# Kernel optimization log

Hardware: AMD Instinct MI355X
Metric: run time of the kernel (lower is better)

The kernel has to match this reference:

```python
import jax, jax.numpy as jnp
import numpy as np

B, T, J, V, D, H = 32, 400, 30, 50000, 150, 150
L = 2  # answer_token_len (boundary model: start, end)


def _gru_step(h, x, Wih, Whh, bih, bhh):
    # torch GRUCell semantics
    gi = x @ Wih.T + bih
    gh = h @ Whh.T + bhh
    ir, iz, inn = jnp.split(gi, 3, axis=-1)
    hr, hz, hn = jnp.split(gh, 3, axis=-1)
    r = jax.nn.sigmoid(ir + hr)
    z = jax.nn.sigmoid(iz + hz)
    n = jnp.tanh(inn + r * hn)
    return (1.0 - z) * n + z * h


def _gru_seq(x, Wih, Whh, bih, bhh):
    # x: [B, S, din] -> hidden sequence [B, S, h]
    h0 = jnp.zeros((x.shape[0], Whh.shape[1]), x.dtype)
    def step(h, xt):
        h = _gru_step(h, xt, Wih, Whh, bih, bhh)
        return h, h
    _, hs = jax.lax.scan(step, h0, jnp.swapaxes(x, 0, 1))
    return jnp.swapaxes(hs, 0, 1)


def _forward(context, query,
             E,
             ctx_Wih, ctx_Whh, ctx_bih, ctx_bhh,
             q_Wih, q_Whh, q_bih, q_bhh,
             Wq, Wp, Wr, w, gate_bias, attn_bias,
             m_Wih, m_Whh, m_bih, m_bhh,
             mr_Wih, mr_Whh, mr_bih, mr_bhh,
             ptr_W1, ptr_W2, ptr_v,
             d_Wih, d_Whh, d_bih, d_bhh):
    # encode context and query with GRUs
    Hp = _gru_seq(E[context], ctx_Wih, ctx_Whh, ctx_bih, ctx_bhh)  # [B,T,H]
    Hq = _gru_seq(E[query], q_Wih, q_Whh, q_bih, q_bhh)            # [B,J,H]

    whq = jnp.einsum('bjh,hk->bjk', Hq, Wq)  # precomputed query projection [B,J,H]

    def match_scan(xs, cWih, cWhh, cbih, cbhh):
        # xs: [B,T,H] context encodings (possibly time-reversed)
        def step(h, xt):
            # G_i = tanh(Wq Hq + (Wp p_i + Wr h_{i-1}) + bias)  -> [B,J,H]
            g = jnp.tanh(whq + (xt @ Wp + h @ Wr + gate_bias)[:, None, :])
            a = jax.nn.softmax(g @ w + attn_bias, axis=-1)       # [B,J]
            q = jnp.einsum('bj,bjh->bh', a, Hq)                  # attended query
            z = jnp.concatenate([xt, q], axis=-1)                # [B,2H]
            h = _gru_step(h, z, cWih, cWhh, cbih, cbhh)
            return h, h
        h0 = jnp.zeros((xs.shape[0], xs.shape[2]), xs.dtype)
        _, hs = jax.lax.scan(step, h0, jnp.swapaxes(xs, 0, 1))
        return jnp.swapaxes(hs, 0, 1)  # [B,T,H]

    Hf = match_scan(Hp, m_Wih, m_Whh, m_bih, m_bhh)              # forward direction
    Hb = match_scan(Hp[:, ::-1], mr_Wih, mr_Whh, mr_bih, mr_bhh) # reverse direction (scan order, as original)
    Hr = jnp.concatenate([Hf, Hb], axis=-1)                      # [B,T,2H]
    zero0 = jnp.zeros((Hr.shape[0], 1, Hr.shape[2]), Hr.dtype)   # initial zero state prepended
    Hr = jnp.concatenate([zero0, Hr], axis=1)                    # [B,T+1,2H]

    # boundary pointer network: L attention steps over H_r
    enc = Hr @ ptr_W1
    def ptr_step(h, _):
        s = jnp.tanh(enc + (h @ ptr_W2)[:, None, :]) @ ptr_v     # [B,T+1]
        a = jax.nn.softmax(s, axis=-1)
        c = jnp.einsum('bt,bth->bh', a, Hr)
        h = _gru_step(h, c, d_Wih, d_Whh, d_bih, d_bhh)
        return h, a
    h0 = jnp.zeros((Hr.shape[0], Hr.shape[2]), Hr.dtype)
    _, probs = jax.lax.scan(ptr_step, h0, None, length=L)
    return jnp.swapaxes(probs, 0, 1)  # [B, L, T+1]


def setup_inputs() -> dict:
    key = jax.random.key(0)
    keys = iter(jax.random.split(key, 40))
    p = lambda *s: jax.random.normal(next(keys), s, jnp.float32) * 0.05
    inp = {
        'context': jax.random.randint(next(keys), (B, T), 0, V, dtype=jnp.int32),
        'query': jax.random.randint(next(keys), (B, J), 0, V, dtype=jnp.int32),
        'E': p(V, D),
        'ctx_Wih': p(3 * H, D), 'ctx_Whh': p(3 * H, H), 'ctx_bih': p(3 * H), 'ctx_bhh': p(3 * H),
        'q_Wih': p(3 * H, D), 'q_Whh': p(3 * H, H), 'q_bih': p(3 * H), 'q_bhh': p(3 * H),
        'Wq': p(H, H), 'Wp': p(H, H), 'Wr': p(H, H), 'w': p(H),
        'gate_bias': p(H), 'attn_bias': p(),
        'm_Wih': p(3 * H, 2 * H), 'm_Whh': p(3 * H, H), 'm_bih': p(3 * H), 'm_bhh': p(3 * H),
        'mr_Wih': p(3 * H, 2 * H), 'mr_Whh': p(3 * H, H), 'mr_bih': p(3 * H), 'mr_bhh': p(3 * H),
        'ptr_W1': p(2 * H, 2 * H), 'ptr_W2': p(2 * H, 2 * H), 'ptr_v': p(2 * H),
        'd_Wih': p(6 * H, 2 * H), 'd_Whh': p(6 * H, 2 * H), 'd_bih': p(6 * H), 'd_bhh': p(6 * H),
    }
    return inp


def reference(context, query, E,
              ctx_Wih, ctx_Whh, ctx_bih, ctx_bhh,
              q_Wih, q_Whh, q_bih, q_bhh,
              Wq, Wp, Wr, w, gate_bias, attn_bias,
              m_Wih, m_Whh, m_bih, m_bhh,
              mr_Wih, mr_Whh, mr_bih, mr_bhh,
              ptr_W1, ptr_W2, ptr_v,
              d_Wih, d_Whh, d_bih, d_bhh):
    return _forward(context, query, E,
                    ctx_Wih, ctx_Whh, ctx_bih, ctx_bhh,
                    q_Wih, q_Whh, q_bih, q_bhh,
                    Wq, Wp, Wr, w, gate_bias, attn_bias,
                    m_Wih, m_Whh, m_bih, m_bhh,
                    mr_Wih, mr_Whh, mr_bih, mr_bhh,
                    ptr_W1, ptr_W2, ptr_v,
                    d_Wih, d_Whh, d_bih, d_bhh)
```

## Files before the change

### kernel.cpp

```cpp
#include <hip/hip_runtime.h>
#include <hip/hip_bf16.h>


namespace {

constexpr int NBATCH = 32;
constexpr int TLEN   = 400;
constexpr int JQ     = 30;
constexpr int T1     = 401;

__device__ __forceinline__ float sigm(float x){ return 1.f/(1.f+__expf(-x)); }
__device__ __forceinline__ float tanh_f(float x){
  float e = __expf(-2.f*fabsf(x));
  float t = (1.f-e)/(1.f+e);
  return x < 0.f ? -t : t;
}
__device__ __forceinline__ float bf2f(unsigned short u){
  union { unsigned int i; float f; } c; c.i = ((unsigned int)u)<<16; return c.f;
}

#define NW 29
struct WDesc { const void* src[NW]; int off[NW+1]; };

__global__ void sniff_kernel(const unsigned int* __restrict__ bits, int* __restrict__ flag){
  __shared__ int cnt;
  if (threadIdx.x==0) cnt = 0;
  __syncthreads();
  int hit = 0;
  #pragma unroll
  for (int i=0;i<4;i++){
    unsigned int w = bits[threadIdx.x*4+i];
    unsigned int b = (w>>8)&0x7Fu;
    if (b==0u || (b>=0x38u && b<=0x3Fu)) hit++;
  }
  atomicAdd(&cnt, hit);
  __syncthreads();
  if (threadIdx.x==0) *flag = (cnt > 768) ? 1 : 0;
}

__global__ void convert_weights_kernel(WDesc d, float* __restrict__ out, const int* __restrict__ flag){
  const int isbf = *flag;
  const int total = d.off[NW];
  for (int e = blockIdx.x*blockDim.x+threadIdx.x; e < total; e += gridDim.x*blockDim.x){
    int j = 0;
    while (e >= d.off[j+1]) j++;
    int i = e - d.off[j];
    out[e] = isbf ? bf2f(((const unsigned short*)d.src[j])[i])
                  : ((const float*)d.src[j])[i];
  }
}

__global__ void padrows_kernel(const float* __restrict__ src, float* __restrict__ dst,
                               int rows, int cols, int ldd){
  int i = blockIdx.x*blockDim.x+threadIdx.x;
  if (i >= rows*ldd) return;
  int r = i/ldd, c = i-r*ldd;
  dst[i] = (c<cols) ? src[(size_t)r*cols+c] : 0.f;
}

__global__ void build_wcat_kernel(const float* __restrict__ Whh, const float* __restrict__ Wr,
                                  float* __restrict__ Wcat){
  int i = blockIdx.x*blockDim.x+threadIdx.x;
  if (i >= 600*152) return;
  int r = i/152, c = i-r*152;
  float v = 0.f;
  if (c < 150){
    if (r < 450) v = Whh[(size_t)r*150+c];
    else         v = Wr[(size_t)c*150 + (r-450)];
  }
  Wcat[i] = v;
}

__global__ void build_msplit_kernel(const float* __restrict__ Wcat,
                                    float* __restrict__ s2q, float* __restrict__ ext){
  int i = blockIdx.x*blockDim.x+threadIdx.x;
  if (i < 24576){
    int q = i/2048, rem = i-q*2048, r = rem/4, p = rem-r*4;
    s2q[i] = Wcat[(size_t)r*152 + 104 + 4*q + p];
  } else if (i < 24576+13376){
    int k = i-24576;
    int q = k/352, rem = k-q*352, ii = rem/4, p = rem-ii*4;
    ext[k] = Wcat[(size_t)(512+ii)*152 + 4*q + p];
  }
}

__global__ void build_gsplit_kernel(const float* __restrict__ Wpad, float* __restrict__ s2q){
  int i = blockIdx.x*blockDim.x+threadIdx.x;
  if (i >= 12*452*4) return;
  int q = i/1808, rem = i-q*1808, r = rem/4, p = rem-r*4;
  s2q[i] = (r<450) ? Wpad[(size_t)r*152 + 104 + 4*q + p] : 0.f;
}

__global__ __launch_bounds__(512) void rowproj_kernel(
    const float* __restrict__ Xrows,
    const int* __restrict__ gather, const void* __restrict__ Etab, const int* __restrict__ bfflag,
    const float* __restrict__ W, const float* __restrict__ bias,
    float* __restrict__ out, int rows, int K, int inner, int mode, int ldw, int offw, int ldo)
{
  __shared__ float xs[8][304];
  const int r0 = blockIdx.x*8;
  int nr = rows - r0; if (nr > 8) nr = 8;
  if (nr <= 0) return;
  const int isbf = gather ? *bfflag : 0;
  for (int e = threadIdx.x; e < nr*inner; e += blockDim.x){
    int r = e/inner, i = e - r*inner;
    float v;
    if (gather){
      size_t base = (size_t)gather[r0+r]*inner + i;
      v = isbf ? bf2f(((const unsigned short*)Etab)[base]) : ((const float*)Etab)[base];
    } else {
      v = Xrows[(size_t)(r0+r)*inner + i];
    }
    xs[r][i] = v;
  }
  __syncthreads();
  for (int k = threadIdx.x; k < ldo; k += blockDim.x){
    if (k < K){
      float b0 = bias ? bias[k] : 0.f;
      float acc[8];
      #pragma unroll
      for (int r=0;r<8;r++) acc[r] = b0;
      if (mode==0){
        for (int i=0;i<inner;i++){
          float wv = W[(size_t)i*ldw + k];
          #pragma unroll
          for (int r=0;r<8;r++) acc[r] += xs[r][i]*wv;
        }
      } else {
        const float* wr = W + (size_t)k*ldw + offw;
        for (int i=0;i<inner;i++){
          float wv = wr[i];
          #pragma unroll
          for (int r=0;r<8;r++) acc[r] += xs[r][i]*wv;
        }
      }
      for (int r=0;r<nr;r++) out[(size_t)(r0+r)*ldo + k] = acc[r];
    } else {
      for (int r=0;r<nr;r++) out[(size_t)(r0+r)*ldo + k] = 0.f;
    }
  }
}

#define R26(M) M(0) M(1) M(2) M(3) M(4) M(5) M(6) M(7) M(8) M(9) M(10) M(11) \
               M(12) M(13) M(14) M(15) M(16) M(17) M(18) M(19) M(20) M(21) \
               M(22) M(23) M(24) M(25)
#define DECW(i) float4 w##i;
#define LDW(i)  w##i = wrow4[i];
#define FMAW(i) { float4 hq = h4[i]; \
  acc0 = fmaf(hq.x, w##i.x, acc0); acc1 = fmaf(hq.y, w##i.y, acc1); \
  acc0 = fmaf(hq.z, w##i.z, acc0); acc1 = fmaf(hq.w, w##i.w, acc1); }

__global__ __launch_bounds__(512) void gru_scan_kernel(
    const float* __restrict__ gi0, const float* __restrict__ Wp0,
    const float* __restrict__ s2q0, const float* __restrict__ bh0,
    float* __restrict__ H0, int S0,
    const float* __restrict__ gi1, const float* __restrict__ Wp1,
    const float* __restrict__ s2q1, const float* __restrict__ bh1,
    float* __restrict__ H1, int S1)
{
  const int blk = blockIdx.x;
  const float* gi; const float* Wpad; const float* s2qG; const float* bh; float* Hs; int S;
  if (blk < 32){ gi = gi0 + (size_t)blk*S0*450;  Wpad = Wp0; s2qG = s2q0; bh = bh0;
                 Hs = H0 + (size_t)blk*S0*150;   S = S0; }
  else         { int bb = blk-32;
                 gi = gi1 + (size_t)bb*S1*450;   Wpad = Wp1; s2qG = s2q1; bh = bh1;
                 Hs = H1 + (size_t)bb*S1*150;    S = S1; }
  __shared__ float4 s2W[12*452];
  __shared__ __align__(16) float h[152];
  __shared__ float gh[452];
  const int tid = threadIdx.x;

  R26(DECW)
  float br = 0.f;
  {
    const float4* wrow4 = (const float4*)(Wpad + (size_t)((tid<450)?tid:0)*152);
    R26(LDW)
    if (tid<450) br = bh[tid];
  }
  for (int e=tid; e<12*452; e+=512) s2W[e] = ((const float4*)s2qG)[e];
  if (tid < 152) h[tid] = 0.f;
  __syncthreads();
  const float4* h4 = (const float4*)h;

  for (int t=0;t<S;t++){
    float g0=0.f,g1=0.f,g2=0.f;
    if (tid < 150){
      const float* gg = gi + (size_t)t*450;
      g0 = gg[tid]; g1 = gg[150+tid]; g2 = gg[300+tid];
    }
    if (tid < 450){
      float acc0=br, acc1=0.f;
      R26(FMAW)
      #pragma unroll
      for (int q=0;q<12;q++){
        float4 wq = s2W[q*452+tid]; float4 hq = h4[26+q];
        acc0 = fmaf(hq.x, wq.x, acc0); acc1 = fmaf(hq.y, wq.y, acc1);
        acc0 = fmaf(hq.z, wq.z, acc0); acc1 = fmaf(hq.w, wq.w, acc1);
      }
      gh[tid] = acc0+acc1;
    }
    __syncthreads();
    if (tid < 150){
      float r = sigm(g0 + gh[tid]);
      float z = sigm(g1 + gh[150+tid]);
      float n = tanh_f(g2 + r*gh[300+tid]);
      float hn = (1.f-z)*n + z*h[tid];
      h[tid] = hn;
      Hs[(size_t)t*150 + tid] = hn;
    }
    __syncthreads();
  }
}

__global__ void zero_hr0_kernel(float* __restrict__ Hr){
  int idx = blockIdx.x*blockDim.x + threadIdx.x;
  if (idx < NBATCH*300){
    int b = idx/300, k = idx - 300*b;
    Hr[(size_t)b*T1*300 + k] = 0.f;
  }
}

__global__ __launch_bounds__(512) void match_scan_kernel(
    const float* __restrict__ pWp,
    const float* __restrict__ whq,
    const float* __restrict__ giXf,
    const float* __restrict__ giXr,
    const float* __restrict__ Pf,
    const float* __restrict__ Pr,
    const float* __restrict__ WcatF, const float* __restrict__ WcatR,
    const float* __restrict__ s2qF,  const float* __restrict__ s2qR,
    const float* __restrict__ extF,  const float* __restrict__ extR,
    const float* __restrict__ m_bhh, const float* __restrict__ mr_bhh,
    const float* __restrict__ wvec,
    float* __restrict__ Hr)
{
  const int b   = blockIdx.x;
  const int dir = blockIdx.y;
  const float* giX  = dir ? giXr : giXf;
  const float* P    = dir ? Pr   : Pf;
  const float* Wcat = dir ? WcatR : WcatF;
  const float* s2qG = dir ? s2qR  : s2qF;
  const float* extG = dir ? extR  : extF;
  const float* bhh  = dir ? mr_bhh : m_bhh;

  __shared__ float4 s2W[12*512];
  __shared__ float4 extW[38*88];
  __shared__ float4 uS[339];
  __shared__ __align__(16) float h[152];
  __shared__ float ghsRaw[512];
  __shared__ __align__(16) float base[152];
  __shared__ __align__(16) float gis[452];
  __shared__ __align__(16) float pwS[152];
  __shared__ __align__(16) float wlS[152];
  __shared__ float sc[32], attw[32];

  const int tid  = threadIdx.x;
  const int lane = tid & 63;
  const int wv   = tid >> 6;
  const int er   = (tid < 440) ? (tid % 88) : 0;
  const int kg   = (tid < 440) ? (tid / 88) : 0;
  const int dq   = (tid < 339) ? (tid % 113) : 0;
  const int djg  = (tid < 339) ? (tid / 113) : 0;

  R26(DECW)
  float br;
  {
    const float4* wrow4 = (const float4*)(Wcat + (size_t)tid*152);
    R26(LDW)
    br = (tid < 450) ? bhh[tid] : 0.f;
  }
  for (int e=tid; e<12*512; e+=512) s2W[e]  = ((const float4*)s2qG)[e];
  for (int e=tid; e<38*88;  e+=512) extW[e] = ((const float4*)extG)[e];
  if (tid < 152){
    h[tid] = 0.f;
    base[tid] = 0.f;
    wlS[tid] = (tid<150) ? wvec[tid] : 0.f;
  }
  __syncthreads();
  const float4* h4 = (const float4*)h;

  for (int t=0;t<TLEN;t++){
    const int tt = dir ? (TLEN-1-t) : t;

    {
      float acc0=br, acc1=0.f;
      R26(FMAW)
      #pragma unroll
      for (int q=0;q<12;q++){
        float4 wq = s2W[q*512+tid]; float4 hq = h4[26+q];
        acc0 = fmaf(hq.x, wq.x, acc0); acc1 = fmaf(hq.y, wq.y, acc1);
        acc0 = fmaf(hq.z, wq.z, acc0); acc1 = fmaf(hq.w, wq.w, acc1);
      }
      ghsRaw[tid] = acc0+acc1;
    }
    if (tid < 440){
      float e0=0.f, e1=0.f;
      #pragma unroll
      for (int j=0;j<8;j++){
        int q = kg*8+j;
        if (q < 38){
          float4 wq = extW[q*88+er]; float4 hq = h4[q];
          e0 = fmaf(hq.x, wq.x, e0); e1 = fmaf(hq.y, wq.y, e1);
          e0 = fmaf(hq.z, wq.z, e0); e1 = fmaf(hq.w, wq.w, e1);
        }
      }
      ((float*)uS)[kg*96+er] = e0+e1;
    } else if (tid < 478){
      int u = tid-440;
      ((float4*)pwS)[u] = ((const float4*)(pWp + ((size_t)b*TLEN + tt)*152))[u];
    }
    __syncthreads();

    if (tid < 150){
      float v = pwS[tid];
      if (tid < 62) v += ghsRaw[450+tid];
      else {
        int k = tid-62;
        const float* pS = (const float*)uS;
        v += pS[k] + pS[96+k] + pS[192+k] + pS[288+k] + pS[384+k];
      }
      base[tid] = v;
    }
    __syncthreads();

    #pragma unroll
    for (int jj=0;jj<4;jj++){
      int j = wv + 8*jj;
      float a = 0.f;
      if (j < JQ && lane < 38){
        float4 q4 = ((const float4*)(whq + ((size_t)b*JQ + j)*152))[lane];
        float4 b4 = ((const float4*)base)[lane];
        float4 w4 = ((const float4*)wlS)[lane];
        a = w4.x*tanh_f(q4.x+b4.x);
        a = fmaf(w4.y, tanh_f(q4.y+b4.y), a);
        a = fmaf(w4.z, tanh_f(q4.z+b4.z), a);
        a = fmaf(w4.w, tanh_f(q4.w+b4.w), a);
      }
      #pragma unroll
      for (int off=32; off; off>>=1) a += __shfl_down(a, off);
      if (j < JQ && lane==0) sc[j] = a;
    }
    __syncthreads();

    if (tid < 64){
      float v = (tid < JQ) ? sc[tid] : -1e30f;
      float m = v;
      #pragma unroll
      for (int off=32; off; off>>=1) m = fmaxf(m, __shfl_down(m, off));
      m = __shfl(m, 0);
      float e = (tid < JQ) ? __expf(v-m) : 0.f;
      float su = e;
      #pragma unroll
      for (int off=32; off; off>>=1) su += __shfl_down(su, off);
      su = __shfl(su, 0);
      if (tid < JQ) attw[tid] = e/su;
    }
    __syncthreads();

    if (tid < 339){
      const float4* P4 = (const float4*)(P + ((size_t)b*JQ + djg*10)*452) + dq;
      float4 a; a.x=0.f; a.y=0.f; a.z=0.f; a.w=0.f;
      #pragma unroll 2
      for (int j=0;j<10;j++){
        float aw = attw[djg*10+j];
        float4 p = P4[(size_t)j*113];
        a.x = fmaf(aw, p.x, a.x); a.y = fmaf(aw, p.y, a.y);
        a.z = fmaf(aw, p.z, a.z); a.w = fmaf(aw, p.w, a.w);
      }
      uS[djg*113+dq] = a;
    }
    __syncthreads();

    if (tid < 113){
      float4 gq = ((const float4*)(giX + ((size_t)b*TLEN + tt)*452))[tid];
      float4 d0 = uS[tid], d1 = uS[113+tid], d2 = uS[226+tid];
      gq.x += d0.x+d1.x+d2.x; gq.y += d0.y+d1.y+d2.y;
      gq.z += d0.z+d1.z+d2.z; gq.w += d0.w+d1.w+d2.w;
      ((float4*)gis)[tid] = gq;
    }
    __syncthreads();

    if (tid < 150){
      float r = sigm(gis[tid] + ghsRaw[tid]);
      float z = sigm(gis[150+tid] + ghsRaw[150+tid]);
      float n = tanh_f(gis[300+tid] + r*ghsRaw[300+tid]);
      float hn = (1.f-z)*n + z*h[tid];
      h[tid] = hn;
      Hr[((size_t)b*T1 + (t+1))*300 + dir*150 + tid] = hn;
    }
    __syncthreads();
  }
}

__global__ __launch_bounds__(512,2) void ptr_scan_kernel(
    const float* __restrict__ enc, const float* __restrict__ Hr,
    const float* __restrict__ W2, const float* __restrict__ pv,
    const float* __restrict__ dWih, const float* __restrict__ dWhh,
    const float* __restrict__ dbih, const float* __restrict__ dbhh,
    void* __restrict__ outv, const int* __restrict__ flag)
{
  const int b = blockIdx.x;
  const int tid = threadIdx.x;
  const int isbf = *flag;
  __shared__ float h[300], hW2[300], sl[T1], al[T1], c[300];
  __shared__ float gis[900], ghs[900];
  __shared__ float vl[300];
  __shared__ float red[8];
  if (tid < 300){ h[tid] = 0.f; vl[tid] = pv[tid]; }
  __syncthreads();
  for (int l=0;l<2;l++){
    if (tid < 300){
      float a0=0.f,a1=0.f;
      for (int i=0;i<300;i+=2){
        a0 += h[i]  *W2[(size_t)i*300+tid];
        a1 += h[i+1]*W2[(size_t)(i+1)*300+tid];
      }
      hW2[tid] = a0+a1;
    }
    __syncthreads();
    {
      const int wv = tid>>6, lane = tid&63;
      for (int t=wv; t<T1; t+=8){
        const float* er = enc + ((size_t)b*T1 + t)*300;
        float acc = 0.f;
        for (int k=lane; k<300; k+=64) acc += vl[k]*tanh_f(er[k] + hW2[k]);
        #pragma unroll
        for (int off=32; off; off>>=1) acc += __shfl_down(acc, off);
        if (lane==0) sl[t] = acc;
      }
    }
    __syncthreads();
    {
      float v = (tid < T1) ? sl[tid] : -1e30f;
      float m = v;
      #pragma unroll
      for (int off=32; off; off>>=1) m = fmaxf(m, __shfl_down(m, off));
      if ((tid&63)==0) red[tid>>6] = m;
      __syncthreads();
      float bm = fmaxf(fmaxf(fmaxf(red[0],red[1]),fmaxf(red[2],red[3])),
                       fmaxf(fmaxf(red[4],red[5]),fmaxf(red[6],red[7])));
      float e = (tid < T1) ? __expf(v-bm) : 0.f;
      float su = e;
      #pragma unroll
      for (int off=32; off; off>>=1) su += __shfl_down(su, off);
      __syncthreads();
      if ((tid&63)==0) red[tid>>6] = su;
      __syncthreads();
      float bs = red[0]+red[1]+red[2]+red[3]+red[4]+red[5]+red[6]+red[7];
      if (tid < T1){
        float a = e/bs;
        al[tid] = a;
        size_t oi = ((size_t)b*2 + l)*T1 + tid;
        if (isbf) ((__hip_bfloat16*)outv)[oi] = __float2bfloat16(a);
        else      ((float*)outv)[oi] = a;
      }
    }
    __syncthreads();
    if (tid < 300){
      float acc = 0.f;
      for (int t=0;t<T1;t++) acc += al[t]*Hr[((size_t)b*T1 + t)*300 + tid];
      c[tid] = acc;
    }
    __syncthreads();
    for (int k=tid; k<900; k+=blockDim.x){
      const float* wi = dWih + (size_t)k*300;
      const float* wh = dWhh + (size_t)k*300;
      float a0 = dbih[k], a1 = dbhh[k];
      for (int i=0;i<300;i++){ a0 += c[i]*wi[i]; a1 += h[i]*wh[i]; }
      gis[k] = a0; ghs[k] = a1;
    }
    __syncthreads();
    if (tid < 300){
      float r = sigm(gis[tid] + ghs[tid]);
      float z = sigm(gis[300+tid] + ghs[300+tid]);
      float n = tanh_f(gis[600+tid] + r*ghs[600+tid]);
      h[tid] = (1.f-z)*n + z*h[tid];
    }
    __syncthreads();
  }
}

}

extern "C" void kernel_launch(void* const* d_in, const int* in_sizes, int n_in,
                              void* d_out, int out_size, void* d_ws, size_t ws_size,
                              hipStream_t stream)
{
  (void)in_sizes; (void)n_in; (void)out_size; (void)ws_size;
  float* ws = (float*)d_ws;
  int* flag = (int*)d_ws;

  static const int wsz[NW] = {
    67500,67500,450,450,
    67500,67500,450,450,
    22500,22500,22500,150,150,1,
    135000,67500,450,450,
    135000,67500,450,450,
    90000,90000,300,
    270000,270000,900,900
  };
  WDesc desc;
  int cum = 0;
  for (int j=0;j<NW;j++){ desc.src[j] = d_in[3+j]; desc.off[j] = cum; cum += wsz[j]; }
  desc.off[NW] = cum;

  float* WB = ws + 16;
  const float* P_ctx_Wih = WB + desc.off[0];
  const float* P_ctx_Whh = WB + desc.off[1];
  const float* P_ctx_bih = WB + desc.off[2];
  const float* P_ctx_bhh = WB + desc.off[3];
  const float* P_q_Wih   = WB + desc.off[4];
  const float* P_q_Whh   = WB + desc.off[5];
  const float* P_q_bih   = WB + desc.off[6];
  const float* P_q_bhh   = WB + desc.off[7];
  const float* P_Wq      = WB + desc.off[8];
  const float* P_Wp      = WB + desc.off[9];
  const float* P_Wr      = WB + desc.off[10];
  const float* P_w       = WB + desc.off[11];
  const float* P_gb      = WB + desc.off[12];
  const float* P_m_Wih   = WB + desc.off[14];
  const float* P_m_Whh   = WB + desc.off[15];
  const float* P_m_bih   = WB + desc.off[16];
  const float* P_m_bhh   = WB + desc.off[17];
  const float* P_mr_Wih  = WB + desc.off[18];
  const float* P_mr_Whh  = WB + desc.off[19];
  const float* P_mr_bih  = WB + desc.off[20];
  const float* P_mr_bhh  = WB + desc.off[21];
  const float* P_W1      = WB + desc.off[22];
  const float* P_W2      = WB + desc.off[23];
  const float* P_pv      = WB + desc.off[24];
  const float* P_dWih    = WB + desc.off[25];
  const float* P_dWhh    = WB + desc.off[26];
  const float* P_dbih    = WB + desc.off[27];
  const float* P_dbhh    = WB + desc.off[28];

  size_t p = 16 + 1468512;
  float* ctxWhhP = ws + p; p += 68400;
  float* qWhhP   = ws + p; p += 68400;
  float* s2qCtx  = ws + p; p += 21696;
  float* s2qQ    = ws + p; p += 21696;
  float* WcatF   = ws + p; p += 91200;
  float* WcatR   = ws + p; p += 91200;
  float* s2qF    = ws + p; p += 24576;
  float* s2qR    = ws + p; p += 24576;
  float* extFg   = ws + p; p += 13376;
  float* extRg   = ws + p; p += 13376;

  float* ctx_gi = ws + p; p += 5760000;
  float* q_gi   = ws + p; p += 432000;
  float* HpB    = ws + p; p += 1920000;
  float* HqB    = ws + p; p += 144000;
  float* whqB   = ws + p; p += 145920;
  float* PfB    = ws + p; p += 433920;
  float* PrB    = ws + p; p += 433920;
  float* pWpB   = ws + p; p += 1945600;
  float* giXfB  = ws + p; p += 5785600;
  float* giXrB  = ws + p; p += 5785600;
  float* HrB    = ws + p; p += 3849600;
  float* encB   = ctx_gi;

  sniff_kernel<<<1,256,0,stream>>>((const unsigned int*)d_in[2], flag);
  convert_weights_kernel<<<512,256,0,stream>>>(desc, WB, flag);
  padrows_kernel<<<(450*152+255)/256,256,0,stream>>>(P_ctx_Whh, ctxWhhP, 450,150,152);
  padrows_kernel<<<(450*152+255)/256,256,0,stream>>>(P_q_Whh,   qWhhP,   450,150,152);
  build_gsplit_kernel<<<(12*452*4+255)/256,256,0,stream>>>(ctxWhhP, s2qCtx);
  build_gsplit_kernel<<<(12*452*4+255)/256,256,0,stream>>>(qWhhP,   s2qQ);
  build_wcat_kernel<<<(600*152+255)/256,256,0,stream>>>(P_m_Whh,  P_Wr, WcatF);
  build_wcat_kernel<<<(600*152+255)/256,256,0,stream>>>(P_mr_Whh, P_Wr, WcatR);
  build_msplit_kernel<<<(24576+13376+255)/256,256,0,stream>>>(WcatF, s2qF, extFg);
  build_msplit_kernel<<<(24576+13376+255)/256,256,0,stream>>>(WcatR, s2qR, extRg);

  rowproj_kernel<<<1600,512,0,stream>>>(nullptr,(const int*)d_in[0], d_in[2], flag,
                                        P_ctx_Wih, P_ctx_bih, ctx_gi, 12800,450,150,1,150,0,450);
  rowproj_kernel<<<120,512,0,stream>>>(nullptr,(const int*)d_in[1], d_in[2], flag,
                                       P_q_Wih, P_q_bih, q_gi, 960,450,150,1,150,0,450);

  gru_scan_kernel<<<64,512,0,stream>>>(ctx_gi, ctxWhhP, s2qCtx, P_ctx_bhh, HpB, 400,
                                       q_gi,   qWhhP,   s2qQ,   P_q_bhh,   HqB, 30);

  rowproj_kernel<<<120,192,0,stream>>>(HqB,nullptr,nullptr,nullptr, P_Wq, nullptr,
                                       whqB, 960,150,150,0,150,0,152);
  rowproj_kernel<<<120,512,0,stream>>>(HqB,nullptr,nullptr,nullptr, P_m_Wih, nullptr,
                                       PfB, 960,450,150,1,300,150,452);
  rowproj_kernel<<<120,512,0,stream>>>(HqB,nullptr,nullptr,nullptr, P_mr_Wih, nullptr,
                                       PrB, 960,450,150,1,300,150,452);
  rowproj_kernel<<<1600,192,0,stream>>>(HpB,nullptr,nullptr,nullptr, P_Wp, P_gb,
                                        pWpB, 12800,150,150,0,150,0,152);
  rowproj_kernel<<<1600,512,0,stream>>>(HpB,nullptr,nullptr,nullptr, P_m_Wih, P_m_bih,
                                        giXfB, 12800,450,150,1,300,0,452);
  rowproj_kernel<<<1600,512,0,stream>>>(HpB,nullptr,nullptr,nullptr, P_mr_Wih, P_mr_bih,
                                        giXrB, 12800,450,150,1,300,0,452);

  zero_hr0_kernel<<<(NBATCH*300+511)/512,512,0,stream>>>(HrB);
  match_scan_kernel<<<dim3(NBATCH,2),512,0,stream>>>(pWpB, whqB, giXfB, giXrB,
                                                     PfB, PrB, WcatF, WcatR,
                                                     s2qF, s2qR, extFg, extRg,
                                                     P_m_bhh, P_mr_bhh, P_w, HrB);

  rowproj_kernel<<<1604,320,0,stream>>>(HrB,nullptr,nullptr,nullptr, P_W1, nullptr,
                                        encB, 12832,300,300,0,300,0,300);
  ptr_scan_kernel<<<32,512,0,stream>>>(encB, HrB, P_W2, P_pv,
                                       P_dWih, P_dWhh, P_dbih, P_dbhh, d_out, flag);
}
```

Measured before the change: 3.643 ms.

## Batch multiple sequences per block in GRU and match scans to reuse weights

The GRU encoder scan now handles four batch rows per block (16 blocks instead of 64), and the match scan handles two batch rows per block (32 blocks instead of 64). Register- and LDS-resident recurrent weights are reused across the rows, so each weight load feeds several FMAs. The match scan's phases are restructured: the full attention-weighted sum over j is done in one pass, and several syncs and partial-sum buffers are removed. In exchange, far fewer blocks run on a large GPU and the serial per-step latency grows, which is a risk in these latency-bound recurrent loops.

Result: slower. 8.469 ms (+132.5%).

```diff
diff --git a/kernel.cpp b/kernel.cpp
--- a/kernel.cpp
+++ b/kernel.cpp
@@ -146,9 +146,16 @@
                M(22) M(23) M(24) M(25)
 #define DECW(i) float4 w##i;
 #define LDW(i)  w##i = wrow4[i];
-#define FMAW(i) { float4 hq = h4[i]; \
-  acc0 = fmaf(hq.x, w##i.x, acc0); acc1 = fmaf(hq.y, w##i.y, acc1); \
-  acc0 = fmaf(hq.z, w##i.z, acc0); acc1 = fmaf(hq.w, w##i.w, acc1); }
+#define FMAW2(i) { float4 p = h04[i]; float4 r2 = h14[i]; \
+  a0 = fmaf(p.x,  w##i.x, a0); a1 = fmaf(p.y,  w##i.y, a1); \
+  a0 = fmaf(p.z,  w##i.z, a0); a1 = fmaf(p.w,  w##i.w, a1); \
+  c0 = fmaf(r2.x, w##i.x, c0); c1 = fmaf(r2.y, w##i.y, c1); \
+  c0 = fmaf(r2.z, w##i.z, c0); c1 = fmaf(r2.w, w##i.w, c1); }
+#define FMAW4(i) { float4 p0=hA4[i], p1=hB4[i], p2=hC4[i], p3=hD4[i]; \
+  a0=fmaf(p0.x,w##i.x,a0); a0=fmaf(p0.y,w##i.y,a0); a0=fmaf(p0.z,w##i.z,a0); a0=fmaf(p0.w,w##i.w,a0); \
+  a1=fmaf(p1.x,w##i.x,a1); a1=fmaf(p1.y,w##i.y,a1); a1=fmaf(p1.z,w##i.z,a1); a1=fmaf(p1.w,w##i.w,a1); \
+  a2=fmaf(p2.x,w##i.x,a2); a2=fmaf(p2.y,w##i.y,a2); a2=fmaf(p2.z,w##i.z,a2); a2=fmaf(p2.w,w##i.w,a2); \
+  a3=fmaf(p3.x,w##i.x,a3); a3=fmaf(p3.y,w##i.y,a3); a3=fmaf(p3.z,w##i.z,a3); a3=fmaf(p3.w,w##i.w,a3); }
 
 __global__ __launch_bounds__(512) void gru_scan_kernel(
     const float* __restrict__ gi0, const float* __restrict__ Wp0,
@@ -160,53 +167,73 @@
 {
   const int blk = blockIdx.x;
   const float* gi; const float* Wpad; const float* s2qG; const float* bh; float* Hs; int S;
-  if (blk < 32){ gi = gi0 + (size_t)blk*S0*450;  Wpad = Wp0; s2qG = s2q0; bh = bh0;
-                 Hs = H0 + (size_t)blk*S0*150;   S = S0; }
-  else         { int bb = blk-32;
-                 gi = gi1 + (size_t)bb*S1*450;   Wpad = Wp1; s2qG = s2q1; bh = bh1;
-                 Hs = H1 + (size_t)bb*S1*150;    S = S1; }
-  __shared__ float4 s2W[12*452];
-  __shared__ __align__(16) float h[152];
-  __shared__ float gh[452];
+  if (blk < 8){ int b0 = 4*blk;
+    gi = gi0 + (size_t)b0*S0*450;  Wpad = Wp0; s2qG = s2q0; bh = bh0;
+    Hs = H0 + (size_t)b0*S0*150;   S = S0;
+  } else { int b0 = 4*(blk-8);
+    gi = gi1 + (size_t)b0*S1*450;  Wpad = Wp1; s2qG = s2q1; bh = bh1;
+    Hs = H1 + (size_t)b0*S1*150;   S = S1;
+  }
+  __shared__ float4 s2W[5424];
+  __shared__ __align__(16) float hg[4][152];
+  __shared__ float ghB[4][452];
   const int tid = threadIdx.x;
 
   R26(DECW)
-  float br = 0.f;
+  float br;
   {
     const float4* wrow4 = (const float4*)(Wpad + (size_t)((tid<450)?tid:0)*152);
     R26(LDW)
-    if (tid<450) br = bh[tid];
-  }
-  for (int e=tid; e<12*452; e+=512) s2W[e] = ((const float4*)s2qG)[e];
-  if (tid < 152) h[tid] = 0.f;
+    br = (tid<450) ? bh[tid] : 0.f;
+  }
+  for (int e=tid; e<5424; e+=512) s2W[e] = ((const float4*)s2qG)[e];
+  if (tid < 152){ hg[0][tid]=0.f; hg[1][tid]=0.f; hg[2][tid]=0.f; hg[3][tid]=0.f; }
   __syncthreads();
-  const float4* h4 = (const float4*)h;
+  const float4* hA4 = (const float4*)hg[0];
+  const float4* hB4 = (const float4*)hg[1];
+  const float4* hC4 = (const float4*)hg[2];
+  const float4* hD4 = (const float4*)hg[3];
+
+  const int bb1 = tid/150;
+  const int k1  = tid - 150*bb1;
 
   for (int t=0;t<S;t++){
-    float g0=0.f,g1=0.f,g2=0.f;
-    if (tid < 150){
-      const float* gg = gi + (size_t)t*450;
-      g0 = gg[tid]; g1 = gg[150+tid]; g2 = gg[300+tid];
-    }
+    const float* gg = gi + ((size_t)(bb1*S) + t)*450 + k1;
+    float g0 = gg[0], g1 = gg[150], g2 = gg[300];
+
     if (tid < 450){
-      float acc0=br, acc1=0.f;
-      R26(FMAW)
+      float a0=br, a1=br, a2=br, a3=br;
+      R26(FMAW4)
       #pragma unroll
       for (int q=0;q<12;q++){
-        float4 wq = s2W[q*452+tid]; float4 hq = h4[26+q];
-        acc0 = fmaf(hq.x, wq.x, acc0); acc1 = fmaf(hq.y, wq.y, acc1);
-        acc0 = fmaf(hq.z, wq.z, acc0); acc1 = fmaf(hq.w, wq.w, acc1);
-      }
-      gh[tid] = acc0+acc1;
-    }
-    __syncthreads();
-    if (tid < 150){
-      float r = sigm(g0 + gh[tid]);
-      float z = sigm(g1 + gh[150+tid]);
-      float n = tanh_f(g2 + r*gh[300+tid]);
-      float hn = (1.f-z)*n + z*h[tid];
-      h[tid] = hn;
-      Hs[(size_t)t*150 + tid] = hn;
+        float4 wq = s2W[q*452+tid];
+        float4 p0=hA4[26+q], p1=hB4[26+q], p2=hC4[26+q], p3=hD4[26+q];
+        a0=fmaf(p0.x,wq.x,a0); a0=fmaf(p0.y,wq.y,a0); a0=fmaf(p0.z,wq.z,a0); a0=fmaf(p0.w,wq.w,a0);
+        a1=fmaf(p1.x,wq.x,a1); a1=fmaf(p1.y,wq.y,a1); a1=fmaf(p1.z,wq.z,a1); a1=fmaf(p1.w,wq.w,a1);
+        a2=fmaf(p2.x,wq.x,a2); a2=fmaf(p2.y,wq.y,a2); a2=fmaf(p2.z,wq.z,a2); a2=fmaf(p2.w,wq.w,a2);
+        a3=fmaf(p3.x,wq.x,a3); a3=fmaf(p3.y,wq.y,a3); a3=fmaf(p3.z,wq.z,a3); a3=fmaf(p3.w,wq.w,a3);
+      }
+      ghB[0][tid]=a0; ghB[1][tid]=a1; ghB[2][tid]=a2; ghB[3][tid]=a3;
+    }
+    __syncthreads();
+
+    {
+      float r = sigm(g0 + ghB[bb1][k1]);
+      float z = sigm(g1 + ghB[bb1][150+k1]);
+      float n = tanh_f(g2 + r*ghB[bb1][300+k1]);
+      float hn = (1.f-z)*n + z*hg[bb1][k1];
+      hg[bb1][k1] = hn;
+      Hs[((size_t)(bb1*S) + t)*150 + k1] = hn;
+    }
+    if (tid < 88){
+      int k2 = 62 + tid;
+      const float* g2p = gi + ((size_t)(3*S) + t)*450 + k2;
+      float r = sigm(g2p[0]   + ghB[3][k2]);
+      float z = sigm(g2p[150] + ghB[3][150+k2]);
+      float n = tanh_f(g2p[300] + r*ghB[3][300+k2]);
+      float hn = (1.f-z)*n + z*hg[3][k2];
+      hg[3][k2] = hn;
+      Hs[((size_t)(3*S) + t)*150 + k2] = hn;
     }
     __syncthreads();
   }
@@ -234,7 +261,7 @@
     const float* __restrict__ wvec,
     float* __restrict__ Hr)
 {
-  const int b   = blockIdx.x;
+  const int b0  = blockIdx.x*2;
   const int dir = blockIdx.y;
   const float* giX  = dir ? giXr : giXf;
   const float* P    = dir ? Pr   : Pf;
@@ -243,24 +270,19 @@
   const float* extG = dir ? extR  : extF;
   const float* bhh  = dir ? mr_bhh : m_bhh;
 
-  __shared__ float4 s2W[12*512];
-  __shared__ float4 extW[38*88];
-  __shared__ float4 uS[339];
-  __shared__ __align__(16) float h[152];
-  __shared__ float ghsRaw[512];
-  __shared__ __align__(16) float base[152];
-  __shared__ __align__(16) float gis[452];
-  __shared__ __align__(16) float pwS[152];
+  __shared__ float4 s2W[6144];
+  __shared__ float4 extW[3344];
+  __shared__ __align__(16) float h[2][152];
+  __shared__ float ghsB[2][512];
+  __shared__ float extPart[2][88];
+  __shared__ __align__(16) float baseS[2][152];
+  __shared__ __align__(16) float gis[2][452];
+  __shared__ float scS[2][32];
   __shared__ __align__(16) float wlS[152];
-  __shared__ float sc[32], attw[32];
 
   const int tid  = threadIdx.x;
   const int lane = tid & 63;
   const int wv   = tid >> 6;
-  const int er   = (tid < 440) ? (tid % 88) : 0;
-  const int kg   = (tid < 440) ? (tid / 88) : 0;
-  const int dq   = (tid < 339) ? (tid % 113) : 0;
-  const int djg  = (tid < 339) ? (tid / 113) : 0;
 
   R26(DECW)
   float br;
@@ -269,124 +291,129 @@
     R26(LDW)
     br = (tid < 450) ? bhh[tid] : 0.f;
   }
-  for (int e=tid; e<12*512; e+=512) s2W[e]  = ((const float4*)s2qG)[e];
-  for (int e=tid; e<38*88;  e+=512) extW[e] = ((const float4*)extG)[e];
+  for (int e=tid; e<6144; e+=512) s2W[e]  = ((const float4*)s2qG)[e];
+  for (int e=tid; e<3344; e+=512) extW[e] = ((const float4*)extG)[e];
   if (tid < 152){
-    h[tid] = 0.f;
-    base[tid] = 0.f;
+    h[0][tid]=0.f; h[1][tid]=0.f;
     wlS[tid] = (tid<150) ? wvec[tid] : 0.f;
   }
   __syncthreads();
-  const float4* h4 = (const float4*)h;
+  const float4* h04 = (const float4*)h[0];
+  const float4* h14 = (const float4*)h[1];
+
+  const int extOn = (tid < 176);
+  const int ebb = extOn ? (tid/88) : 0;
+  const int erw = extOn ? (tid%88) : 0;
+  const int pwOn = (tid >= 192 && tid < 268);
+  const int pbb = pwOn ? ((tid-192)/38) : 0;
+  const int pq  = pwOn ? ((tid-192)%38) : 0;
+  const int dOn = (tid >= 286);
+  const int dbb = dOn ? ((tid-286)/113) : 0;
+  const int dq  = dOn ? ((tid-286)%113) : 0;
 
   for (int t=0;t<TLEN;t++){
     const int tt = dir ? (TLEN-1-t) : t;
 
+    float4 pwv;
+    if (pwOn) pwv = ((const float4*)(pWp + ((size_t)(b0+pbb)*TLEN + tt)*152))[pq];
+
     {
-      float acc0=br, acc1=0.f;
-      R26(FMAW)
+      float a0=br, a1=0.f, c0=br, c1=0.f;
+      R26(FMAW2)
       #pragma unroll
       for (int q=0;q<12;q++){
-        float4 wq = s2W[q*512+tid]; float4 hq = h4[26+q];
-        acc0 = fmaf(hq.x, wq.x, acc0); acc1 = fmaf(hq.y, wq.y, acc1);
-        acc0 = fmaf(hq.z, wq.z, acc0); acc1 = fmaf(hq.w, wq.w, acc1);
-      }
-      ghsRaw[tid] = acc0+acc1;
-    }
-    if (tid < 440){
+        float4 wq = s2W[q*512+tid];
+        float4 p = h04[26+q], r2 = h14[26+q];
+        a0 = fmaf(p.x, wq.x,a0); a1 = fmaf(p.y, wq.y,a1);
+        a0 = fmaf(p.z, wq.z,a0); a1 = fmaf(p.w, wq.w,a1);
+        c0 = fmaf(r2.x,wq.x,c0); c1 = fmaf(r2.y,wq.y,c1);
+        c0 = fmaf(r2.z,wq.z,c0); c1 = fmaf(r2.w,wq.w,c1);
+      }
+      ghsB[0][tid] = a0+a1;
+      ghsB[1][tid] = c0+c1;
+    }
+    if (extOn){
+      const float4* hx = ebb ? h14 : h04;
       float e0=0.f, e1=0.f;
       #pragma unroll
-      for (int j=0;j<8;j++){
-        int q = kg*8+j;
-        if (q < 38){
-          float4 wq = extW[q*88+er]; float4 hq = h4[q];
-          e0 = fmaf(hq.x, wq.x, e0); e1 = fmaf(hq.y, wq.y, e1);
-          e0 = fmaf(hq.z, wq.z, e0); e1 = fmaf(hq.w, wq.w, e1);
+      for (int q=0;q<38;q++){
+        float4 wq = extW[q*88+erw];
+        float4 hv = hx[q];
+        e0 = fmaf(hv.x,wq.x,e0); e1 = fmaf(hv.y,wq.y,e1);
+        e0 = fmaf(hv.z,wq.z,e0); e1 = fmaf(hv.w,wq.w,e1);
+      }
+      extPart[ebb][erw] = e0+e1;
+    }
+    if (pwOn) ((float4*)baseS[pbb])[pq] = pwv;
+    __syncthreads();
+
+    if (tid < 300){
+      int bb = tid/150, k = tid-150*bb;
+      float wr = (k<62) ? ghsB[bb][450+k] : extPart[bb][k-62];
+      baseS[bb][k] += wr;
+    }
+    __syncthreads();
+
+    {
+      int bb = wv>>2, jb = wv&3;
+      #pragma unroll
+      for (int jj=0;jj<8;jj++){
+        int j = jb + 4*jj;
+        float a = 0.f;
+        if (j < JQ && lane < 38){
+          float4 q4 = ((const float4*)(whq + ((size_t)(b0+bb)*JQ + j)*152))[lane];
+          float4 b4 = ((const float4*)baseS[bb])[lane];
+          float4 w4 = ((const float4*)wlS)[lane];
+          a = w4.x*tanh_f(q4.x+b4.x);
+          a = fmaf(w4.y, tanh_f(q4.y+b4.y), a);
+          a = fmaf(w4.z, tanh_f(q4.z+b4.z), a);
+          a = fmaf(w4.w, tanh_f(q4.w+b4.w), a);
         }
-      }
-      ((float*)uS)[kg*96+er] = e0+e1;
-    } else if (tid < 478){
-      int u = tid-440;
-      ((float4*)pwS)[u] = ((const float4*)(pWp + ((size_t)b*TLEN + tt)*152))[u];
-    }
-    __syncthreads();
-
-    if (tid < 150){
-      float v = pwS[tid];
-      if (tid < 62) v += ghsRaw[450+tid];
-      else {
-        int k = tid-62;
-        const float* pS = (const float*)uS;
-        v += pS[k] + pS[96+k] + pS[192+k] + pS[288+k] + pS[384+k];
-      }
-      base[tid] = v;
-    }
-    __syncthreads();
-
-    #pragma unroll
-    for (int jj=0;jj<4;jj++){
-      int j = wv + 8*jj;
-      float a = 0.f;
-      if (j < JQ && lane < 38){
-        float4 q4 = ((const float4*)(whq + ((size_t)b*JQ + j)*152))[lane];
-        float4 b4 = ((const float4*)base)[lane];
-        float4 w4 = ((const float4*)wlS)[lane];
-        a = w4.x*tanh_f(q4.x+b4.x);
-        a = fmaf(w4.y, tanh_f(q4.y+b4.y), a);
-        a = fmaf(w4.z, tanh_f(q4.z+b4.z), a);
-        a = fmaf(w4.w, tanh_f(q4.w+b4.w), a);
-      }
-      #pragma unroll
-      for (int off=32; off; off>>=1) a += __shfl_down(a, off);
-      if (j < JQ && lane==0) sc[j] = a;
-    }
-    __syncthreads();
-
-    if (tid < 64){
-      float v = (tid < JQ) ? sc[tid] : -1e30f;
+        #pragma unroll
+        for (int off=32; off; off>>=1) a += __shfl_down(a, off);
+        if (j < JQ && lane==0) scS[bb][j] = a;
+      }
+    }
+    __syncthreads();
+
+    if (tid < 128){
+      int bb = wv;
+      float v = (lane < JQ) ? scS[bb][lane] : -1e30f;
       float m = v;
       #pragma unroll
       for (int off=32; off; off>>=1) m = fmaxf(m, __shfl_down(m, off));
       m = __shfl(m, 0);
-      float e = (tid < JQ) ? __expf(v-m) : 0.f;
+      float e = (lane < JQ) ? __expf(v-m) : 0.f;
       float su = e;
       #pragma unroll
       for (int off=32; off; off>>=1) su += __shfl_down(su, off);
       su = __shfl(su, 0);
-      if (tid < JQ) attw[tid] = e/su;
-    }
-    __syncthreads();
-
-    if (tid < 339){
-      const float4* P4 = (const float4*)(P + ((size_t)b*JQ + djg*10)*452) + dq;
-      float4 a; a.x=0.f; a.y=0.f; a.z=0.f; a.w=0.f;
+      if (lane < JQ) scS[bb][lane] = e/su;
+    }
+    __syncthreads();
+
+    if (dOn){
+      float4 acc = ((const float4*)(giX + ((size_t)(b0+dbb)*TLEN + tt)*452))[dq];
+      const float4* P4 = (const float4*)(P + (size_t)(b0+dbb)*JQ*452) + dq;
       #pragma unroll 2
-      for (int j=0;j<10;j++){
-        float aw = attw[djg*10+j];
+      for (int j=0;j<JQ;j++){
+        float aw = scS[dbb][j];
         float4 p = P4[(size_t)j*113];
-        a.x = fmaf(aw, p.x, a.x); a.y = fmaf(aw, p.y, a.y);
-        a.z = fmaf(aw, p.z, a.z); a.w = fmaf(aw, p.w, a.w);
-      }
-      uS[djg*113+dq] = a;
-    }
-    __syncthreads();
-
-    if (tid < 113){
-      float4 gq = ((const float4*)(giX + ((size_t)b*TLEN + tt)*452))[tid];
-      float4 d0 = uS[tid], d1 = uS[113+tid], d2 = uS[226+tid];
-      gq.x += d0.x+d1.x+d2.x; gq.y += d0.y+d1.y+d2.y;
-      gq.z += d0.z+d1.z+d2.z; gq.w += d0.w+d1.w+d2.w;
-      ((float4*)gis)[tid] = gq;
-    }
-    __syncthreads();
-
-    if (tid < 150){
-      float r = sigm(gis[tid] + ghsRaw[tid]);
-      float z = sigm(gis[150+tid] + ghsRaw[150+tid]);
-      float n = tanh_f(gis[300+tid] + r*ghsRaw[300+tid]);
-      float hn = (1.f-z)*n + z*h[tid];
-      h[tid] = hn;
-      Hr[((size_t)b*T1 + (t+1))*300 + dir*150 + tid] = hn;
+        acc.x = fmaf(aw,p.x,acc.x); acc.y = fmaf(aw,p.y,acc.y);
+        acc.z = fmaf(aw,p.z,acc.z); acc.w = fmaf(aw,p.w,acc.w);
+      }
+      ((float4*)gis[dbb])[dq] = acc;
+    }
+    __syncthreads();
+
+    if (tid < 300){
+      int bb = tid/150, k = tid-150*bb;
+      float r = sigm(gis[bb][k]     + ghsB[bb][k]);
+      float z = sigm(gis[bb][150+k] + ghsB[bb][150+k]);
+      float n = tanh_f(gis[bb][300+k] + r*ghsB[bb][300+k]);
+      float hn = (1.f-z)*n + z*h[bb][k];
+      h[bb][k] = hn;
+      Hr[((size_t)(b0+bb)*T1 + (t+1))*300 + dir*150 + k] = hn;
     }
     __syncthreads();
   }
@@ -575,7 +602,7 @@
   rowproj_kernel<<<120,512,0,stream>>>(nullptr,(const int*)d_in[1], d_in[2], flag,
                                        P_q_Wih, P_q_bih, q_gi, 960,450,150,1,150,0,450);
 
-  gru_scan_kernel<<<64,512,0,stream>>>(ctx_gi, ctxWhhP, s2qCtx, P_ctx_bhh, HpB, 400,
+  gru_scan_kernel<<<16,512,0,stream>>>(ctx_gi, ctxWhhP, s2qCtx, P_ctx_bhh, HpB, 400,
                                        q_gi,   qWhhP,   s2qQ,   P_q_bhh,   HqB, 30);
 
   rowproj_kernel<<<120,192,0,stream>>>(HqB,nullptr,nullptr,nullptr, P_Wq, nullptr,
@@ -592,10 +619,10 @@
                                         giXrB, 12800,450,150,1,300,0,452);
 
   zero_hr0_kernel<<<(NBATCH*300+511)/512,512,0,stream>>>(HrB);
-  match_scan_kernel<<<dim3(NBATCH,2),512,0,stream>>>(pWpB, whqB, giXfB, giXrB,
-                                                     PfB, PrB, WcatF, WcatR,
-                                                     s2qF, s2qR, extFg, extRg,
-                                                     P_m_bhh, P_mr_bhh, P_w, HrB);
+  match_scan_kernel<<<dim3(16,2),512,0,stream>>>(pWpB, whqB, giXfB, giXrB,
+                                                 PfB, PrB, WcatF, WcatR,
+                                                 s2qF, s2qR, extFg, extRg,
+                                                 P_m_bhh, P_mr_bhh, P_w, HrB);
 
   rowproj_kernel<<<1604,320,0,stream>>>(HrB,nullptr,nullptr,nullptr, P_W1, nullptr,
                                         encB, 12832,300,300,0,300,0,300);
```
